# Kernel tuning notes

Hardware: AMD Instinct MI355X
Metric: run time of the kernel (lower is better)

The kernel has to match this reference:

```python
import jax, jax.numpy as jnp
import numpy as np

N = 100000   # nodes
E = 1600000  # edges
F = 128      # num_features
D = 64       # embedding_size
G = 512      # graphs in batch


def setup_inputs() -> dict:
    key = jax.random.key(0)
    ks = jax.random.split(key, 10)
    x = jax.random.normal(ks[0], (N, F), jnp.float32)
    edge_index = jax.random.randint(ks[1], (2, E), 0, N, jnp.int32)
    batch_index = jnp.sort(jax.random.randint(ks[2], (N,), 0, G, jnp.int32))
    s = lambda i, sh: jax.random.normal(ks[i], sh, jnp.float32) * 0.1
    return dict(
        x=x, edge_index=edge_index, batch_index=batch_index, num_graphs=G,
        W0=s(3, (F, D)), b0=jnp.zeros((D,), jnp.float32),
        W1=s(4, (D, D)), b1=jnp.zeros((D,), jnp.float32),
        W2=s(5, (D, D)), b2=jnp.zeros((D,), jnp.float32),
        W3=s(6, (D, D)), b3=jnp.zeros((D,), jnp.float32),
        Wout=s(7, (2 * D, 1)), bout=jnp.zeros((1,), jnp.float32),
    )


def _gcn_prep(edge_index, n):
    # add self loops, compute symmetric degree normalization (PyG gcn_norm)
    loop = jnp.arange(n, dtype=edge_index.dtype)
    src = jnp.concatenate([edge_index[0], loop])
    dst = jnp.concatenate([edge_index[1], loop])
    deg = jax.ops.segment_sum(jnp.ones_like(dst, jnp.float32), dst, num_segments=n)
    dinv = jnp.where(deg > 0, jax.lax.rsqrt(deg), 0.0)
    norm = dinv[src] * dinv[dst]  # [E+N]
    return src, dst, norm


def _gcn_conv(x, W, b, src, dst, norm, n):
    h = x @ W                                   # [N, D] transform first (small D)
    msgs = h[src] * norm[:, None]               # gather + degree-normalize
    out = jax.ops.segment_sum(msgs, dst, num_segments=n)  # scatter-add
    return out + b


def reference(x, edge_index, batch_index, num_graphs,
              W0, b0, W1, b1, W2, b2, W3, b3, Wout, bout):
    n = x.shape[0]
    src, dst, norm = _gcn_prep(edge_index, n)
    h = jnp.tanh(_gcn_conv(x, W0, b0, src, dst, norm, n))
    h = jnp.tanh(_gcn_conv(h, W1, b1, src, dst, norm, n))
    h = jnp.tanh(_gcn_conv(h, W2, b2, src, dst, norm, n))
    h = jnp.tanh(_gcn_conv(h, W3, b3, src, dst, norm, n))
    # global max pool + global mean pool over batch_index
    counts = jax.ops.segment_sum(jnp.ones((n,), jnp.float32), batch_index,
                                 num_segments=num_graphs)
    maxp = jax.ops.segment_max(h, batch_index, num_segments=num_graphs)
    maxp = jnp.where(counts[:, None] > 0, maxp, 0.0)
    meanp = jax.ops.segment_sum(h, batch_index, num_segments=num_graphs) \
        / jnp.maximum(counts, 1.0)[:, None]
    hidden = jnp.concatenate([maxp, meanp], axis=1)  # [G, 2D]
    out = jax.nn.sigmoid(hidden @ Wout + bout)       # [G, 1]
    return out, hidden
```

## Files before the change

### kernel.cpp

```cpp
#include <hip/hip_runtime.h>
#include <math.h>
#include <float.h>

#define NN 100000
#define EE 1600000
#define FF 128
#define DD 64
#define GG 512
#define NBLK 98
#define WPASS 25000

__device__ __forceinline__ unsigned short f2bf(float f) {
    unsigned u = __float_as_uint(f);
    u = (u + 0x7fff + ((u >> 16) & 1)) >> 16;
    return (unsigned short)u;
}
__device__ __forceinline__ float bflo(unsigned u) { return __uint_as_float(u << 16); }
__device__ __forceinline__ float bfhi(unsigned u) { return __uint_as_float(u & 0xffff0000u); }

__global__ void init_deg(int* degi) {
    int i = blockIdx.x * 256 + threadIdx.x;
    if (i < NN) degi[i] = 1;
}

__global__ void edge_deg(const int* __restrict__ dst, int* degi) {
    int e = blockIdx.x * 256 + threadIdx.x;
    if (e < EE) atomicAdd(&degi[dst[e]], 1);
}

__global__ void make_dinv(const int* __restrict__ degi, float* __restrict__ dinv) {
    int i = blockIdx.x * 256 + threadIdx.x;
    if (i < NN) dinv[i] = rsqrtf((float)degi[i]);
}

__global__ void scan_partial(const int* __restrict__ degi, int* __restrict__ partial) {
    __shared__ int red[1024];
    int tid = threadIdx.x;
    int idx = blockIdx.x * 1024 + tid;
    red[tid] = (idx < NN) ? degi[idx] - 1 : 0;
    __syncthreads();
    #pragma unroll
    for (int off = 512; off; off >>= 1) {
        if (tid < off) red[tid] += red[tid + off];
        __syncthreads();
    }
    if (tid == 0) partial[blockIdx.x] = red[0];
}

__global__ void scan_offsets(int* __restrict__ partial, int* __restrict__ row_ptr) {
    __shared__ int tmp[128];
    int tid = threadIdx.x;
    int v = (tid < NBLK) ? partial[tid] : 0;
    tmp[tid] = v;
    __syncthreads();
    #pragma unroll
    for (int off = 1; off < 128; off <<= 1) {
        int t = (tid >= off) ? tmp[tid - off] : 0;
        __syncthreads();
        tmp[tid] += t;
        __syncthreads();
    }
    if (tid < NBLK) partial[tid] = tmp[tid] - v;
    if (tid == NBLK - 1) row_ptr[NN] = tmp[tid];
}

__global__ void scan_final(const int* __restrict__ degi, const int* __restrict__ partial,
                           int* __restrict__ row_ptr, int* __restrict__ cursor) {
    __shared__ int tmp[1024];
    int tid = threadIdx.x;
    int idx = blockIdx.x * 1024 + tid;
    int v = (idx < NN) ? degi[idx] - 1 : 0;
    tmp[tid] = v;
    __syncthreads();
    #pragma unroll
    for (int off = 1; off < 1024; off <<= 1) {
        int t = (tid >= off) ? tmp[tid - off] : 0;
        __syncthreads();
        tmp[tid] += t;
        __syncthreads();
    }
    int excl = partial[blockIdx.x] + tmp[tid] - v;
    if (idx < NN) { row_ptr[idx] = excl; cursor[idx] = excl; }
}

__global__ void fill_csr_win(const int* __restrict__ src, const int* __restrict__ dst,
                             const float* __restrict__ dinv,
                             int* __restrict__ cursor, int2* __restrict__ cw, int lo) {
    int e = blockIdx.x * 256 + threadIdx.x;
    if (e < EE) {
        int v = dst[e];
        if ((unsigned)(v - lo) < WPASS) {
            int u = src[e];
            int pos = atomicAdd(&cursor[v], 1);
            float w = dinv[u] * dinv[v];
            cw[pos] = make_int2(u, __float_as_int(w));
        }
    }
}

template <int K>
__global__ __launch_bounds__(256) void gemm_k(const float* __restrict__ X,
                                              const float* __restrict__ W,
                                              unsigned short* __restrict__ T2) {
    __shared__ float sX[64 * 65];
    __shared__ float sW[64 * 64];
    int tid = threadIdx.x;
    int row0 = blockIdx.x * 64;
    int rows = NN - row0; if (rows > 64) rows = 64;
    int r0 = (tid >> 4) << 2;
    int c0 = (tid & 15) << 2;
    float acc[4][4] = {};
    for (int k0 = 0; k0 < K; k0 += 64) {
        {
            const float4* Wg = (const float4*)(W + (size_t)k0 * 64);
            float4* sW4 = (float4*)sW;
            #pragma unroll
            for (int j = 0; j < 4; ++j) sW4[tid + j * 256] = Wg[tid + j * 256];
        }
        #pragma unroll
        for (int j = 0; j < 4; ++j) {
            int flat = tid + j * 256;
            int r = flat >> 4, kc = (flat & 15) << 2;
            float4 v = make_float4(0.f, 0.f, 0.f, 0.f);
            if (r < rows) v = *(const float4*)(X + (size_t)(row0 + r) * K + k0 + kc);
            sX[r * 65 + kc]     = v.x;
            sX[r * 65 + kc + 1] = v.y;
            sX[r * 65 + kc + 2] = v.z;
            sX[r * 65 + kc + 3] = v.w;
        }
        __syncthreads();
        #pragma unroll 8
        for (int k = 0; k < 64; ++k) {
            float4 b = *(const float4*)(sW + k * 64 + c0);
            float a0 = sX[r0 * 65 + k];
            float a1 = sX[(r0 + 1) * 65 + k];
            float a2 = sX[(r0 + 2) * 65 + k];
            float a3 = sX[(r0 + 3) * 65 + k];
            acc[0][0] = fmaf(a0, b.x, acc[0][0]); acc[0][1] = fmaf(a0, b.y, acc[0][1]);
            acc[0][2] = fmaf(a0, b.z, acc[0][2]); acc[0][3] = fmaf(a0, b.w, acc[0][3]);
            acc[1][0] = fmaf(a1, b.x, acc[1][0]); acc[1][1] = fmaf(a1, b.y, acc[1][1]);
            acc[1][2] = fmaf(a1, b.z, acc[1][2]); acc[1][3] = fmaf(a1, b.w, acc[1][3]);
            acc[2][0] = fmaf(a2, b.x, acc[2][0]); acc[2][1] = fmaf(a2, b.y, acc[2][1]);
            acc[2][2] = fmaf(a2, b.z, acc[2][2]); acc[2][3] = fmaf(a2, b.w, acc[2][3]);
            acc[3][0] = fmaf(a3, b.x, acc[3][0]); acc[3][1] = fmaf(a3, b.y, acc[3][1]);
            acc[3][2] = fmaf(a3, b.z, acc[3][2]); acc[3][3] = fmaf(a3, b.w, acc[3][3]);
        }
        __syncthreads();
    }
    #pragma unroll
    for (int i = 0; i < 4; ++i) {
        int r = row0 + r0 + i;
        if (r < NN) {
            ushort4 o;
            o.x = f2bf(acc[i][0]); o.y = f2bf(acc[i][1]);
            o.z = f2bf(acc[i][2]); o.w = f2bf(acc[i][3]);
            *(ushort4*)(T2 + (size_t)r * 64 + c0) = o;
        }
    }
}

__global__ __launch_bounds__(256) void agg_k(const uint4* __restrict__ T4,
                                             const float* __restrict__ dinv,
                                             const int* __restrict__ row_ptr,
                                             const int2* __restrict__ cw,
                                             const float* __restrict__ bias,
                                             float4* __restrict__ A4) {
    int node = blockIdx.x * 4 + (threadIdx.x >> 6);
    int lane = threadIdx.x & 63;
    int grp  = lane >> 3;
    int fl   = lane & 7;
    int beg = row_ptr[node], end = row_ptr[node + 1];
    float a0=0,a1=0,a2=0,a3=0,a4=0,a5=0,a6=0,a7=0;
    int j = beg + grp;
    for (; j + 24 < end; j += 32) {
        int2 c1 = cw[j];
        int2 c2 = cw[j + 8];
        int2 c3 = cw[j + 16];
        int2 c4 = cw[j + 24];
        uint4 t1 = T4[(size_t)c1.x * 8 + fl];
        uint4 t2 = T4[(size_t)c2.x * 8 + fl];
        uint4 t3 = T4[(size_t)c3.x * 8 + fl];
        uint4 t4 = T4[(size_t)c4.x * 8 + fl];
        float w1 = __int_as_float(c1.y);
        float w2 = __int_as_float(c2.y);
        float w3 = __int_as_float(c3.y);
        float w4 = __int_as_float(c4.y);
        a0 = fmaf(bflo(t1.x), w1, a0); a1 = fmaf(bfhi(t1.x), w1, a1);
        a2 = fmaf(bflo(t1.y), w1, a2); a3 = fmaf(bfhi(t1.y), w1, a3);
        a4 = fmaf(bflo(t1.z), w1, a4); a5 = fmaf(bfhi(t1.z), w1, a5);
        a6 = fmaf(bflo(t1.w), w1, a6); a7 = fmaf(bfhi(t1.w), w1, a7);
        a0 = fmaf(bflo(t2.x), w2, a0); a1 = fmaf(bfhi(t2.x), w2, a1);
        a2 = fmaf(bflo(t2.y), w2, a2); a3 = fmaf(bfhi(t2.y), w2, a3);
        a4 = fmaf(bflo(t2.z), w2, a4); a5 = fmaf(bfhi(t2.z), w2, a5);
        a6 = fmaf(bflo(t2.w), w2, a6); a7 = fmaf(bfhi(t2.w), w2, a7);
        a0 = fmaf(bflo(t3.x), w3, a0); a1 = fmaf(bfhi(t3.x), w3, a1);
        a2 = fmaf(bflo(t3.y), w3, a2); a3 = fmaf(bfhi(t3.y), w3, a3);
        a4 = fmaf(bflo(t3.z), w3, a4); a5 = fmaf(bfhi(t3.z), w3, a5);
        a6 = fmaf(bflo(t3.w), w3, a6); a7 = fmaf(bfhi(t3.w), w3, a7);
        a0 = fmaf(bflo(t4.x), w4, a0); a1 = fmaf(bfhi(t4.x), w4, a1);
        a2 = fmaf(bflo(t4.y), w4, a2); a3 = fmaf(bfhi(t4.y), w4, a3);
        a4 = fmaf(bflo(t4.z), w4, a4); a5 = fmaf(bfhi(t4.z), w4, a5);
        a6 = fmaf(bflo(t4.w), w4, a6); a7 = fmaf(bfhi(t4.w), w4, a7);
    }
    for (; j < end; j += 8) {
        int2 c = cw[j];
        float w = __int_as_float(c.y);
        uint4 t = T4[(size_t)c.x * 8 + fl];
        a0 = fmaf(bflo(t.x), w, a0); a1 = fmaf(bfhi(t.x), w, a1);
        a2 = fmaf(bflo(t.y), w, a2); a3 = fmaf(bfhi(t.y), w, a3);
        a4 = fmaf(bflo(t.z), w, a4); a5 = fmaf(bfhi(t.z), w, a5);
        a6 = fmaf(bflo(t.w), w, a6); a7 = fmaf(bfhi(t.w), w, a7);
    }
    #pragma unroll
    for (int m = 8; m <= 32; m <<= 1) {
        a0 += __shfl_xor(a0, m); a1 += __shfl_xor(a1, m);
        a2 += __shfl_xor(a2, m); a3 += __shfl_xor(a3, m);
        a4 += __shfl_xor(a4, m); a5 += __shfl_xor(a5, m);
        a6 += __shfl_xor(a6, m); a7 += __shfl_xor(a7, m);
    }
    if (grp == 0) {
        float dv = dinv[node];
        float s = dv * dv;
        uint4 t = T4[(size_t)node * 8 + fl];
        const float* b = &bias[fl * 8];
        float4 o0, o1;
        o0.x = tanhf(fmaf(bflo(t.x), s, a0) + b[0]);
        o0.y = tanhf(fmaf(bfhi(t.x), s, a1) + b[1]);
        o0.z = tanhf(fmaf(bflo(t.y), s, a2) + b[2]);
        o0.w = tanhf(fmaf(bfhi(t.y), s, a3) + b[3]);
        o1.x = tanhf(fmaf(bflo(t.z), s, a4) + b[4]);
        o1.y = tanhf(fmaf(bfhi(t.z), s, a5) + b[5]);
        o1.z = tanhf(fmaf(bflo(t.w), s, a6) + b[6]);
        o1.w = tanhf(fmaf(bfhi(t.w), s, a7) + b[7]);
        A4[(size_t)node * 16 + fl * 2]     = o0;
        A4[(size_t)node * 16 + fl * 2 + 1] = o1;
    }
}

__global__ void find_bounds(const int* __restrict__ batch, int* __restrict__ gstart) {
    int i = blockIdx.x * 256 + threadIdx.x;
    if (i >= NN) return;
    int cur = batch[i];
    int prev = (i == 0) ? -1 : batch[i - 1];
    for (int g = prev + 1; g <= cur; ++g) gstart[g] = i;
    if (i == NN - 1) {
        for (int g = cur + 1; g <= GG; ++g) gstart[g] = NN;
    }
}

__global__ __launch_bounds__(256) void pool_k(const float* __restrict__ H,
                                              const int* __restrict__ gstart,
                                              float* __restrict__ hidden) {
    __shared__ float smax[4][64], ssum[4][64];
    int g = blockIdx.x;
    int wave = threadIdx.x >> 6, lane = threadIdx.x & 63;
    int beg = gstart[g], end = gstart[g + 1];
    float mx = -FLT_MAX, sm = 0.f;
    for (int i = beg + wave; i < end; i += 4) {
        float v = H[(size_t)i * 64 + lane];
        mx = fmaxf(mx, v);
        sm += v;
    }
    smax[wave][lane] = mx; ssum[wave][lane] = sm;
    __syncthreads();
    if (wave == 0) {
        mx = fmaxf(fmaxf(smax[0][lane], smax[1][lane]), fmaxf(smax[2][lane], smax[3][lane]));
        sm = ssum[0][lane] + ssum[1][lane] + ssum[2][lane] + ssum[3][lane];
        int cnt = end - beg;
        hidden[g * 128 + lane]      = (cnt > 0) ? mx : 0.f;
        hidden[g * 128 + 64 + lane] = sm / fmaxf((float)cnt, 1.f);
    }
}

__global__ void head_k(const float* __restrict__ hidden, const float* __restrict__ Wout,
                       const float* __restrict__ bout, float* __restrict__ out) {
    int g = blockIdx.x, lane = threadIdx.x;
    float v = hidden[g * 128 + lane] * Wout[lane]
            + hidden[g * 128 + 64 + lane] * Wout[64 + lane];
    #pragma unroll
    for (int off = 32; off; off >>= 1) v += __shfl_down(v, off);
    if (lane == 0) out[g] = 1.f / (1.f + expf(-(v + bout[0])));
}

extern "C" void kernel_launch(void* const* d_in, const int* in_sizes, int n_in,
                              void* d_out, int out_size, void* d_ws, size_t ws_size,
                              hipStream_t stream) {
    const float* x     = (const float*)d_in[0];
    const int*   ei    = (const int*)d_in[1];
    const int*   src   = ei;
    const int*   dst   = ei + EE;
    const int*   batch = (const int*)d_in[2];
    const float* W0 = (const float*)d_in[4];  const float* b0 = (const float*)d_in[5];
    const float* W1 = (const float*)d_in[6];  const float* b1 = (const float*)d_in[7];
    const float* W2 = (const float*)d_in[8];  const float* b2 = (const float*)d_in[9];
    const float* W3 = (const float*)d_in[10]; const float* b3 = (const float*)d_in[11];
    const float* Wout = (const float*)d_in[12]; const float* bout = (const float*)d_in[13];

    float* out    = (float*)d_out;
    float* hidden = out + GG;

    char*  w = (char*)d_ws;
    size_t off = 0;
    auto alloc = [&](size_t bytes) -> char* {
        char* p = w + off;
        off = (off + bytes + 255) & ~(size_t)255;
        return p;
    };
    int*   degi    = (int*)  alloc(NN * 4);
    float* dinv    = (float*)alloc(NN * 4);
    int*   row_ptr = (int*)  alloc((NN + 1) * 4);
    int*   cursor  = (int*)  alloc(NN * 4);
    int*   partial = (int*)  alloc(NBLK * 4);
    int2*  cw      = (int2*) alloc((size_t)EE * 8);
    unsigned short* T2 = (unsigned short*)alloc((size_t)NN * 64 * 2);
    float* A       = (float*)alloc((size_t)NN * 64 * 4);
    int*   gstart  = (int*)  alloc((GG + 1) * 4);
    (void)ws_size; (void)in_sizes; (void)n_in; (void)out_size;

    init_deg<<<(NN + 255) / 256, 256, 0, stream>>>(degi);
    edge_deg<<<(EE + 255) / 256, 256, 0, stream>>>(dst, degi);
    scan_partial<<<NBLK, 1024, 0, stream>>>(degi, partial);
    scan_offsets<<<1, 128, 0, stream>>>(partial, row_ptr);
    scan_final<<<NBLK, 1024, 0, stream>>>(degi, partial, row_ptr, cursor);
    make_dinv<<<(NN + 255) / 256, 256, 0, stream>>>(degi, dinv);
    for (int lo = 0; lo < NN; lo += WPASS)
        fill_csr_win<<<(EE + 255) / 256, 256, 0, stream>>>(src, dst, dinv, cursor, cw, lo);

    find_bounds<<<(NN + 255) / 256, 256, 0, stream>>>(batch, gstart);

    const int GB = (NN + 63) / 64;
    gemm_k<FF><<<GB, 256, 0, stream>>>(x, W0, T2);
    agg_k<<<NN / 4, 256, 0, stream>>>((const uint4*)T2, dinv, row_ptr, cw, b0, (float4*)A);
    gemm_k<DD><<<GB, 256, 0, stream>>>(A, W1, T2);
    agg_k<<<NN / 4, 256, 0, stream>>>((const uint4*)T2, dinv, row_ptr, cw, b1, (float4*)A);
    gemm_k<DD><<<GB, 256, 0, stream>>>(A, W2, T2);
    agg_k<<<NN / 4, 256, 0, stream>>>((const uint4*)T2, dinv, row_ptr, cw, b2, (float4*)A);
    gemm_k<DD><<<GB, 256, 0, stream>>>(A, W3, T2);
    agg_k<<<NN / 4, 256, 0, stream>>>((const uint4*)T2, dinv, row_ptr, cw, b3, (float4*)A);

    pool_k<<<GG, 256, 0, stream>>>(A, gstart, hidden);
    head_k<<<GG, 64, 0, stream>>>(hidden, Wout, bout, out);
}
```

Measured before the change: 666.3 us.

## Use bf16 MFMA GEMMs, store activations as bf16, fill CSR in one pass

The scalar fp32 tiled GEMM is replaced by a kernel that stages inputs and transposed weights as bf16 in shared memory and computes 16x16x32 bf16 MFMA tiles. The aggregation output is now packed bf16, which halves activation write/read traffic for the next GEMM and for pooling. The four windowed CSR fill passes become a single pass. Element-wise shared loads and scalar bf16 stores in the GEMM, plus extra bf16 rounding of activations, add accuracy risk. Dropping the windowing may also lose the locality of atomics and scattered writes that it was meant to provide.

```diff
diff --git a/kernel.cpp b/kernel.cpp
--- a/kernel.cpp
+++ b/kernel.cpp
@@ -8,7 +8,9 @@
 #define DD 64
 #define GG 512
 #define NBLK 98
-#define WPASS 25000
+
+typedef __attribute__((ext_vector_type(8))) short bf16x8;
+typedef __attribute__((ext_vector_type(4))) float f32x4;
 
 __device__ __forceinline__ unsigned short f2bf(float f) {
     unsigned u = __float_as_uint(f);
@@ -17,6 +19,7 @@
 }
 __device__ __forceinline__ float bflo(unsigned u) { return __uint_as_float(u << 16); }
 __device__ __forceinline__ float bfhi(unsigned u) { return __uint_as_float(u & 0xffff0000u); }
+__device__ __forceinline__ float bfs(unsigned short u) { return __uint_as_float((unsigned)u << 16); }
 
 __global__ void init_deg(int* degi) {
     int i = blockIdx.x * 256 + threadIdx.x;
@@ -83,78 +86,68 @@
     if (idx < NN) { row_ptr[idx] = excl; cursor[idx] = excl; }
 }
 
-__global__ void fill_csr_win(const int* __restrict__ src, const int* __restrict__ dst,
-                             const float* __restrict__ dinv,
-                             int* __restrict__ cursor, int2* __restrict__ cw, int lo) {
+__global__ void fill_csr(const int* __restrict__ src, const int* __restrict__ dst,
+                         const float* __restrict__ dinv,
+                         int* __restrict__ cursor, int2* __restrict__ cw) {
     int e = blockIdx.x * 256 + threadIdx.x;
     if (e < EE) {
-        int v = dst[e];
-        if ((unsigned)(v - lo) < WPASS) {
-            int u = src[e];
-            int pos = atomicAdd(&cursor[v], 1);
-            float w = dinv[u] * dinv[v];
-            cw[pos] = make_int2(u, __float_as_int(w));
-        }
-    }
-}
-
-template <int K>
-__global__ __launch_bounds__(256) void gemm_k(const float* __restrict__ X,
-                                              const float* __restrict__ W,
-                                              unsigned short* __restrict__ T2) {
-    __shared__ float sX[64 * 65];
-    __shared__ float sW[64 * 64];
+        int u = src[e], v = dst[e];
+        int pos = atomicAdd(&cursor[v], 1);
+        float w = dinv[u] * dinv[v];
+        cw[pos] = make_int2(u, __float_as_int(w));
+    }
+}
+
+template <int K, typename InT>
+__global__ __launch_bounds__(256) void gemm_mfma(const InT* __restrict__ X,
+                                                 const float* __restrict__ W,
+                                                 unsigned short* __restrict__ T2) {
+    constexpr int KP = K + 8;
+    __shared__ unsigned short sA[64 * KP];
+    __shared__ unsigned short sWt[64 * KP];
     int tid = threadIdx.x;
     int row0 = blockIdx.x * 64;
-    int rows = NN - row0; if (rows > 64) rows = 64;
-    int r0 = (tid >> 4) << 2;
-    int c0 = (tid & 15) << 2;
-    float acc[4][4] = {};
-    for (int k0 = 0; k0 < K; k0 += 64) {
-        {
-            const float4* Wg = (const float4*)(W + (size_t)k0 * 64);
-            float4* sW4 = (float4*)sW;
-            #pragma unroll
-            for (int j = 0; j < 4; ++j) sW4[tid + j * 256] = Wg[tid + j * 256];
+
+    for (int i = tid; i < K * 64; i += 256) {
+        int k = i >> 6, c = i & 63;
+        sWt[c * KP + k] = f2bf(W[k * 64 + c]);
+    }
+    for (int i = tid; i < 64 * K; i += 256) {
+        int r = i / K, k = i % K;
+        int gr = row0 + r;
+        unsigned short v = 0;
+        if (gr < NN) {
+            if constexpr (sizeof(InT) == 4) v = f2bf((float)X[(size_t)gr * K + k]);
+            else                            v = (unsigned short)X[(size_t)gr * K + k];
         }
-        #pragma unroll
-        for (int j = 0; j < 4; ++j) {
-            int flat = tid + j * 256;
-            int r = flat >> 4, kc = (flat & 15) << 2;
-            float4 v = make_float4(0.f, 0.f, 0.f, 0.f);
-            if (r < rows) v = *(const float4*)(X + (size_t)(row0 + r) * K + k0 + kc);
-            sX[r * 65 + kc]     = v.x;
-            sX[r * 65 + kc + 1] = v.y;
-            sX[r * 65 + kc + 2] = v.z;
-            sX[r * 65 + kc + 3] = v.w;
-        }
-        __syncthreads();
-        #pragma unroll 8
-        for (int k = 0; k < 64; ++k) {
-            float4 b = *(const float4*)(sW + k * 64 + c0);
-            float a0 = sX[r0 * 65 + k];
-            float a1 = sX[(r0 + 1) * 65 + k];
-            float a2 = sX[(r0 + 2) * 65 + k];
-            float a3 = sX[(r0 + 3) * 65 + k];
-            acc[0][0] = fmaf(a0, b.x, acc[0][0]); acc[0][1] = fmaf(a0, b.y, acc[0][1]);
-            acc[0][2] = fmaf(a0, b.z, acc[0][2]); acc[0][3] = fmaf(a0, b.w, acc[0][3]);
-            acc[1][0] = fmaf(a1, b.x, acc[1][0]); acc[1][1] = fmaf(a1, b.y, acc[1][1]);
-            acc[1][2] = fmaf(a1, b.z, acc[1][2]); acc[1][3] = fmaf(a1, b.w, acc[1][3]);
-            acc[2][0] = fmaf(a2, b.x, acc[2][0]); acc[2][1] = fmaf(a2, b.y, acc[2][1]);
-            acc[2][2] = fmaf(a2, b.z, acc[2][2]); acc[2][3] = fmaf(a2, b.w, acc[2][3]);
-            acc[3][0] = fmaf(a3, b.x, acc[3][0]); acc[3][1] = fmaf(a3, b.y, acc[3][1]);
-            acc[3][2] = fmaf(a3, b.z, acc[3][2]); acc[3][3] = fmaf(a3, b.w, acc[3][3]);
-        }
-        __syncthreads();
-    }
-    #pragma unroll
-    for (int i = 0; i < 4; ++i) {
-        int r = row0 + r0 + i;
+        sA[r * KP + k] = v;
+    }
+    __syncthreads();
+
+    int wv = tid >> 6, l = tid & 63;
+    int tr = l & 15;
+    int kq = (l >> 4) * 8;
+    const unsigned short* pA = sA + (wv * 16 + tr) * KP + kq;
+    const unsigned short* pB = sWt + tr * KP + kq;
+    f32x4 a0 = {0,0,0,0}, a1 = {0,0,0,0}, a2 = {0,0,0,0}, a3 = {0,0,0,0};
+    #pragma unroll
+    for (int k0 = 0; k0 < K; k0 += 32) {
+        bf16x8 af = *(const bf16x8*)(pA + k0);
+        a0 = __builtin_amdgcn_mfma_f32_16x16x32_bf16(af, *(const bf16x8*)(pB + 0 * 16 * KP + k0), a0, 0, 0, 0);
+        a1 = __builtin_amdgcn_mfma_f32_16x16x32_bf16(af, *(const bf16x8*)(pB + 1 * 16 * KP + k0), a1, 0, 0, 0);
+        a2 = __builtin_amdgcn_mfma_f32_16x16x32_bf16(af, *(const bf16x8*)(pB + 2 * 16 * KP + k0), a2, 0, 0, 0);
+        a3 = __builtin_amdgcn_mfma_f32_16x16x32_bf16(af, *(const bf16x8*)(pB + 3 * 16 * KP + k0), a3, 0, 0, 0);
+    }
+    int orow0 = row0 + wv * 16 + (l >> 4) * 4;
+    #pragma unroll
+    for (int reg = 0; reg < 4; ++reg) {
+        int r = orow0 + reg;
         if (r < NN) {
-            ushort4 o;
-            o.x = f2bf(acc[i][0]); o.y = f2bf(acc[i][1]);
-            o.z = f2bf(acc[i][2]); o.w = f2bf(acc[i][3]);
-            *(ushort4*)(T2 + (size_t)r * 64 + c0) = o;
+            size_t base = (size_t)r * 64 + tr;
+            T2[base]      = f2bf(a0[reg]);
+            T2[base + 16] = f2bf(a1[reg]);
+            T2[base + 32] = f2bf(a2[reg]);
+            T2[base + 48] = f2bf(a3[reg]);
         }
     }
 }
@@ -164,7 +157,7 @@
                                              const int* __restrict__ row_ptr,
                                              const int2* __restrict__ cw,
                                              const float* __restrict__ bias,
-                                             float4* __restrict__ A4) {
+                                             uint4* __restrict__ A4) {
     int node = blockIdx.x * 4 + (threadIdx.x >> 6);
     int lane = threadIdx.x & 63;
     int grp  = lane >> 3;
@@ -223,17 +216,20 @@
         float s = dv * dv;
         uint4 t = T4[(size_t)node * 8 + fl];
         const float* b = &bias[fl * 8];
-        float4 o0, o1;
-        o0.x = tanhf(fmaf(bflo(t.x), s, a0) + b[0]);
-        o0.y = tanhf(fmaf(bfhi(t.x), s, a1) + b[1]);
-        o0.z = tanhf(fmaf(bflo(t.y), s, a2) + b[2]);
-        o0.w = tanhf(fmaf(bfhi(t.y), s, a3) + b[3]);
-        o1.x = tanhf(fmaf(bflo(t.z), s, a4) + b[4]);
-        o1.y = tanhf(fmaf(bfhi(t.z), s, a5) + b[5]);
-        o1.z = tanhf(fmaf(bflo(t.w), s, a6) + b[6]);
-        o1.w = tanhf(fmaf(bfhi(t.w), s, a7) + b[7]);
-        A4[(size_t)node * 16 + fl * 2]     = o0;
-        A4[(size_t)node * 16 + fl * 2 + 1] = o1;
+        float v0 = tanhf(fmaf(bflo(t.x), s, a0) + b[0]);
+        float v1 = tanhf(fmaf(bfhi(t.x), s, a1) + b[1]);
+        float v2 = tanhf(fmaf(bflo(t.y), s, a2) + b[2]);
+        float v3 = tanhf(fmaf(bfhi(t.y), s, a3) + b[3]);
+        float v4 = tanhf(fmaf(bflo(t.z), s, a4) + b[4]);
+        float v5 = tanhf(fmaf(bfhi(t.z), s, a5) + b[5]);
+        float v6 = tanhf(fmaf(bflo(t.w), s, a6) + b[6]);
+        float v7 = tanhf(fmaf(bfhi(t.w), s, a7) + b[7]);
+        uint4 o;
+        o.x = (unsigned)f2bf(v0) | ((unsigned)f2bf(v1) << 16);
+        o.y = (unsigned)f2bf(v2) | ((unsigned)f2bf(v3) << 16);
+        o.z = (unsigned)f2bf(v4) | ((unsigned)f2bf(v5) << 16);
+        o.w = (unsigned)f2bf(v6) | ((unsigned)f2bf(v7) << 16);
+        A4[(size_t)node * 8 + fl] = o;
     }
 }
 
@@ -248,7 +244,7 @@
     }
 }
 
-__global__ __launch_bounds__(256) void pool_k(const float* __restrict__ H,
+__global__ __launch_bounds__(256) void pool_k(const unsigned short* __restrict__ H2,
                                               const int* __restrict__ gstart,
                                               float* __restrict__ hidden) {
     __shared__ float smax[4][64], ssum[4][64];
@@ -257,7 +253,7 @@
     int beg = gstart[g], end = gstart[g + 1];
     float mx = -FLT_MAX, sm = 0.f;
     for (int i = beg + wave; i < end; i += 4) {
-        float v = H[(size_t)i * 64 + lane];
+        float v = bfs(H2[(size_t)i * 64 + lane]);
         mx = fmaxf(mx, v);
         sm += v;
     }
@@ -313,7 +309,7 @@
     int*   partial = (int*)  alloc(NBLK * 4);
     int2*  cw      = (int2*) alloc((size_t)EE * 8);
     unsigned short* T2 = (unsigned short*)alloc((size_t)NN * 64 * 2);
-    float* A       = (float*)alloc((size_t)NN * 64 * 4);
+    unsigned short* A2 = (unsigned short*)alloc((size_t)NN * 64 * 2);
     int*   gstart  = (int*)  alloc((GG + 1) * 4);
     (void)ws_size; (void)in_sizes; (void)n_in; (void)out_size;
 
@@ -323,21 +319,20 @@
     scan_offsets<<<1, 128, 0, stream>>>(partial, row_ptr);
     scan_final<<<NBLK, 1024, 0, stream>>>(degi, partial, row_ptr, cursor);
     make_dinv<<<(NN + 255) / 256, 256, 0, stream>>>(degi, dinv);
-    for (int lo = 0; lo < NN; lo += WPASS)
-        fill_csr_win<<<(EE + 255) / 256, 256, 0, stream>>>(src, dst, dinv, cursor, cw, lo);
+    fill_csr<<<(EE + 255) / 256, 256, 0, stream>>>(src, dst, dinv, cursor, cw);
 
     find_bounds<<<(NN + 255) / 256, 256, 0, stream>>>(batch, gstart);
 
     const int GB = (NN + 63) / 64;
-    gemm_k<FF><<<GB, 256, 0, stream>>>(x, W0, T2);
-    agg_k<<<NN / 4, 256, 0, stream>>>((const uint4*)T2, dinv, row_ptr, cw, b0, (float4*)A);
-    gemm_k<DD><<<GB, 256, 0, stream>>>(A, W1, T2);
-    agg_k<<<NN / 4, 256, 0, stream>>>((const uint4*)T2, dinv, row_ptr, cw, b1, (float4*)A);
-    gemm_k<DD><<<GB, 256, 0, stream>>>(A, W2, T2);
-    agg_k<<<NN / 4, 256, 0, stream>>>((const uint4*)T2, dinv, row_ptr, cw, b2, (float4*)A);
-    gemm_k<DD><<<GB, 256, 0, stream>>>(A, W3, T2);
-    agg_k<<<NN / 4, 256, 0, stream>>>((const uint4*)T2, dinv, row_ptr, cw, b3, (float4*)A);
-
-    pool_k<<<GG, 256, 0, stream>>>(A, gstart, hidden);
+    gemm_mfma<FF, float><<<GB, 256, 0, stream>>>(x, W0, T2);
+    agg_k<<<NN / 4, 256, 0, stream>>>((const uint4*)T2, dinv, row_ptr, cw, b0, (uint4*)A2);
+    gemm_mfma<DD, unsigned short><<<GB, 256, 0, stream>>>(A2, W1, T2);
+    agg_k<<<NN / 4, 256, 0, stream>>>((const uint4*)T2, dinv, row_ptr, cw, b1, (uint4*)A2);
+    gemm_mfma<DD, unsigned short><<<GB, 256, 0, stream>>>(A2, W2, T2);
+    agg_k<<<NN / 4, 256, 0, stream>>>((const uint4*)T2, dinv, row_ptr, cw, b2, (uint4*)A2);
+    gemm_mfma<DD, unsigned short><<<GB, 256, 0, stream>>>(A2, W3, T2);
+    agg_k<<<NN / 4, 256, 0, stream>>>((const uint4*)T2, dinv, row_ptr, cw, b3, (uint4*)A2);
+
+    pool_k<<<GG, 256, 0, stream>>>(A2, gstart, hidden);
     head_k<<<GG, 64, 0, stream>>>(hidden, Wout, bout, out);
 }
```

Measured after the change: 649.2 us. -2.6%, faster.
